# Optimization experiments

Measured on AMD Instinct MI355X. Metric: run time of the kernel, lower is better.

## Reference

```python
import jax, jax.numpy as jnp
import numpy as np
import math


def setup_inputs() -> dict:
    key0 = jax.random.key(0)
    kq, kk, kv = jax.random.split(key0, 3)
    B, H, L, S, D = 2, 8, 2048, 2048, 64
    query = jax.random.normal(kq, (B, H, L, D), dtype=jnp.float32)
    key = jax.random.normal(kk, (B, H, S, D), dtype=jnp.float32)
    value = jax.random.normal(kv, (B, H, S, D), dtype=jnp.float32)
    return {"query": query, "key": key, "value": value}


def reference(query, key, value):
    # SDPA with last=True, attn_mask=None, is_causal=False, dropout_p=0.0,
    # hook_fn is a side-effect callback whose return value is unused -> no-op.
    D = query.shape[-1]
    scale_factor = 1.0 / math.sqrt(D)
    # [B, H, L, S] attention scores
    attn_weight = jnp.einsum("bhld,bhsd->bhls", query, key) * scale_factor
    # last=True branch: self-similarity softmaxes of q and k
    q_attn = jnp.einsum("bhld,bhmd->bhlm", query, query) * scale_factor
    k_attn = jnp.einsum("bhsd,bhtd->bhst", key, key) * scale_factor
    output_attn_weight = jax.nn.softmax(q_attn, axis=-1) + jax.nn.softmax(k_attn, axis=-1)
    attn_weight = jax.nn.softmax(attn_weight, axis=-1)
    # dropout_p = 0.0 -> identity
    out = jnp.einsum("bhls,bhsd->bhld", attn_weight, value)
    return (out, output_attn_weight)
```

## Files before the change

### kernel.cpp

```cpp
#include <hip/hip_runtime.h>
#include <hip/hip_bf16.h>

#define LL 2048
#define DD 64

typedef __attribute__((ext_vector_type(4))) float f32x4;
typedef __attribute__((ext_vector_type(8))) short short8;
typedef __attribute__((ext_vector_type(4))) short short4v;

#define S1 0.18033688011112042f
#define S2 23.083120654223414f

static __device__ __forceinline__ short f2bf(float f) {
    union { float f; unsigned u; } v; v.f = f;
    unsigned r = v.u + 0x7fffu + ((v.u >> 16) & 1u);
    return (short)(r >> 16);
}

__global__ __launch_bounds__(256)
void prep_cvt(const float* __restrict__ Q, const float* __restrict__ K,
              short* __restrict__ Qb, short* __restrict__ Kb) {
    const float* src = blockIdx.y ? K : Q;
    short* dst = blockIdx.y ? Kb : Qb;
    size_t i = ((size_t)blockIdx.x * 256 + threadIdx.x) * 4;
    f32x4 v = *(const f32x4*)(src + i);
    short4v o;
    o[0] = f2bf(v[0]); o[1] = f2bf(v[1]); o[2] = f2bf(v[2]); o[3] = f2bf(v[3]);
    *(short4v*)(dst + i) = o;
}

__global__ __launch_bounds__(256)
void prep_vt(const float* __restrict__ V, short* __restrict__ Vt) {
    const int bh = blockIdx.y;
    const int s0 = blockIdx.x * 64;
    const int sl = threadIdx.x & 63;
    const int d0 = threadIdx.x >> 6;
    const float* Vs = V + (size_t)bh * LL * DD;
    short* Vd = Vt + (size_t)bh * DD * LL;
#pragma unroll
    for (int i = 0; i < 16; ++i) {
        int d = d0 + i * 4;
        Vd[(size_t)d * LL + s0 + sl] = f2bf(Vs[(size_t)(s0 + sl) * DD + d]);
    }
}


__global__ __launch_bounds__(512, 4)
void attnw_sums(const short* __restrict__ Qb, const short* __restrict__ Kb,
                float* __restrict__ Ssum) {
    const int bh = blockIdx.y;
    const int mat = blockIdx.z;
    const int r0 = blockIdx.x * 128;
    const int tid = threadIdx.x;
    const int lane = tid & 63;
    const int wid = tid >> 6;
    const int q = lane >> 4;
    const int c0 = lane & 15;

    __shared__ short8 stg[512];

    const short* X = (mat ? Kb : Qb) + (size_t)bh * LL * DD;
    float* Sd = Ssum + ((size_t)mat * 16 + bh) * LL;

    const int rw = r0 + wid * 16;
    const short8 a0 = *(const short8*)(X + (size_t)(rw + c0) * DD + q * 8);
    const short8 a1 = *(const short8*)(X + (size_t)(rw + c0) * DD + 32 + q * 8);

    const int sc = tid >> 3;
    const int sd = tid & 7;
    const int sslot = sc * 8 + (sd ^ (sc & 7));

    float sum[4] = {0.f, 0.f, 0.f, 0.f};
    short8 rst = *(const short8*)(X + (size_t)sc * DD + sd * 8);
    for (int i = 0; i < 32; ++i) {
        __syncthreads();
        stg[sslot] = rst;
        __syncthreads();
        if (i + 1 < 32)
            rst = *(const short8*)(X + (size_t)((i + 1) * 64 + sc) * DD + sd * 8);
#pragma unroll
        for (int h = 0; h < 4; ++h) {
            const int col = h * 16 + c0;
            short8 b0 = stg[col * 8 + (q ^ (c0 & 7))];
            short8 b1 = stg[col * 8 + ((q + 4) ^ (c0 & 7))];
            f32x4 z = {0.f, 0.f, 0.f, 0.f};
            z = __builtin_amdgcn_mfma_f32_16x16x32_bf16(a0, b0, z, 0, 0, 0);
            z = __builtin_amdgcn_mfma_f32_16x16x32_bf16(a1, b1, z, 0, 0, 0);
#pragma unroll
            for (int r = 0; r < 4; ++r)
                sum[r] += __builtin_amdgcn_exp2f(z[r] * S1 - S2);
        }
    }
#pragma unroll
    for (int off = 1; off < 16; off <<= 1)
#pragma unroll
        for (int r = 0; r < 4; ++r) sum[r] += __shfl_xor(sum[r], off, 64);
    if (c0 == 0) {
#pragma unroll
        for (int r = 0; r < 4; ++r) Sd[rw + q * 4 + r] = sum[r];
    }
}

__global__ __launch_bounds__(256, 4)
void attnw_write(const short* __restrict__ Qb, const short* __restrict__ Kb,
                 const float* __restrict__ Ssum, float* __restrict__ out2) {
    const int bh = blockIdx.y;
    const int r0 = blockIdx.x * 64;
    const int tid = threadIdx.x;
    const int lane = tid & 63;
    const int wid = tid >> 6;
    const int q = lane >> 4;
    const int c0 = lane & 15;

    __shared__ short8 stgQ[256];
    __shared__ short8 stgK[256];
    __shared__ __align__(16) float ob[4][16][36];

    const short* Qh = Qb + (size_t)bh * LL * DD;
    const short* Kh = Kb + (size_t)bh * LL * DD;
    const float* Sq = Ssum + (size_t)bh * LL;
    const float* Sk = Ssum + (size_t)(16 + bh) * LL;

    const int rw = r0 + wid * 16;
    const short8 aq0 = *(const short8*)(Qh + (size_t)(rw + c0) * DD + q * 8);
    const short8 aq1 = *(const short8*)(Qh + (size_t)(rw + c0) * DD + 32 + q * 8);
    const short8 ak0 = *(const short8*)(Kh + (size_t)(rw + c0) * DD + q * 8);
    const short8 ak1 = *(const short8*)(Kh + (size_t)(rw + c0) * DD + 32 + q * 8);

    float rclQ[4], rclK[4];
#pragma unroll
    for (int r = 0; r < 4; ++r) {
        rclQ[r] = 1.0f / Sq[rw + q * 4 + r];
        rclK[r] = 1.0f / Sk[rw + q * 4 + r];
    }

    const int sc = tid >> 3;
    const int sd = tid & 7;
    const int sslot = sc * 8 + (sd ^ (sc & 7));

    float* outp = out2 + (size_t)bh * LL * LL + (size_t)rw * LL;

    short8 rq = *(const short8*)(Qh + (size_t)sc * DD + sd * 8);
    short8 rk = *(const short8*)(Kh + (size_t)sc * DD + sd * 8);
    for (int i = 0; i < 64; ++i) {
        __syncthreads();
        stgQ[sslot] = rq;
        stgK[sslot] = rk;
        __syncthreads();
        if (i + 1 < 64) {
            rq = *(const short8*)(Qh + (size_t)((i + 1) * 32 + sc) * DD + sd * 8);
            rk = *(const short8*)(Kh + (size_t)((i + 1) * 32 + sc) * DD + sd * 8);
        }
#pragma unroll
        for (int h = 0; h < 2; ++h) {
            const int col = h * 16 + c0;
            short8 bq0 = stgQ[col * 8 + (q ^ (c0 & 7))];
            short8 bq1 = stgQ[col * 8 + ((q + 4) ^ (c0 & 7))];
            short8 bk0 = stgK[col * 8 + (q ^ (c0 & 7))];
            short8 bk1 = stgK[col * 8 + ((q + 4) ^ (c0 & 7))];
            f32x4 zq = {0.f, 0.f, 0.f, 0.f}, zk = {0.f, 0.f, 0.f, 0.f};
            zq = __builtin_amdgcn_mfma_f32_16x16x32_bf16(aq0, bq0, zq, 0, 0, 0);
            zq = __builtin_amdgcn_mfma_f32_16x16x32_bf16(aq1, bq1, zq, 0, 0, 0);
            zk = __builtin_amdgcn_mfma_f32_16x16x32_bf16(ak0, bk0, zk, 0, 0, 0);
            zk = __builtin_amdgcn_mfma_f32_16x16x32_bf16(ak1, bk1, zk, 0, 0, 0);
#pragma unroll
            for (int r = 0; r < 4; ++r) {
                float v = __builtin_amdgcn_exp2f(zq[r] * S1 - S2) * rclQ[r]
                        + __builtin_amdgcn_exp2f(zk[r] * S1 - S2) * rclK[r];
                ob[wid][q * 4 + r][h * 16 + c0] = v;
            }
        }
#pragma unroll
        for (int j = 0; j < 2; ++j) {
            int idx = lane + j * 64;
            int row = idx >> 3;
            int c8 = idx & 7;
            f32x4 v = *(const f32x4*)(&ob[wid][row][c8 * 4]);
            __builtin_nontemporal_store(
                v, (f32x4*)&outp[(size_t)row * LL + i * 32 + c8 * 4]);
        }
    }
}

__global__ __launch_bounds__(256, 4)
void sdpa_kernel(const short* __restrict__ Qb, const short* __restrict__ Kb,
                 const short* __restrict__ Vt, float* __restrict__ out1) {
    const int bh = blockIdx.y;
    const int r0 = blockIdx.x * 16;
    const int tid = threadIdx.x;
    const int lane = tid & 63;
    const int cw = tid >> 6;
    const int q = lane >> 4;
    const int c0 = lane & 15;
    const int colbase = cw * 512;

    __shared__ float redsum[4][16];
    __shared__ __align__(16) short pbuf[4][16][40];
    __shared__ float obuf[4][1024];

    const short* Qh = Qb + (size_t)bh * LL * DD;
    const short* Kh = Kb + (size_t)bh * LL * DD;
    const short* Vh = Vt + (size_t)bh * DD * LL;

    const short8 a0 = *(const short8*)(Qh + (size_t)(r0 + c0) * DD + q * 8);
    const short8 a1 = *(const short8*)(Qh + (size_t)(r0 + c0) * DD + 32 + q * 8);

    f32x4 oacc[4];
#pragma unroll
    for (int dt = 0; dt < 4; ++dt) { f32x4 z = {0.f,0.f,0.f,0.f}; oacc[dt] = z; }
    float sum[4] = {0.f, 0.f, 0.f, 0.f};

#pragma unroll 4
    for (int sb = 0; sb < 16; ++sb) {
        const int sglob = colbase + sb * 32;
#pragma unroll
        for (int h = 0; h < 2; ++h) {
            const short* Bp = Kh + (size_t)(sglob + h * 16 + c0) * DD + q * 8;
            short8 b0 = *(const short8*)Bp;
            short8 b1 = *(const short8*)(Bp + 32);
            f32x4 z = {0.f, 0.f, 0.f, 0.f};
            z = __builtin_amdgcn_mfma_f32_16x16x32_bf16(a0, b0, z, 0, 0, 0);
            z = __builtin_amdgcn_mfma_f32_16x16x32_bf16(a1, b1, z, 0, 0, 0);
#pragma unroll
            for (int r = 0; r < 4; ++r) {
                float e = __builtin_amdgcn_exp2f(z[r] * S1);
                sum[r] += e;
                pbuf[cw][q * 4 + r][h * 16 + c0] = f2bf(e);
            }
        }
        short8 ap = *(const short8*)(&pbuf[cw][c0][q * 8]);
#pragma unroll
        for (int dt = 0; dt < 4; ++dt) {
            short8 bv = *(const short8*)(Vh + (size_t)(dt * 16 + c0) * LL + sglob + q * 8);
            oacc[dt] = __builtin_amdgcn_mfma_f32_16x16x32_bf16(ap, bv, oacc[dt], 0, 0, 0);
        }
    }

#pragma unroll
    for (int off = 1; off < 16; off <<= 1)
#pragma unroll
        for (int r = 0; r < 4; ++r) sum[r] += __shfl_xor(sum[r], off, 64);
    if (c0 == 0) {
#pragma unroll
        for (int r = 0; r < 4; ++r) redsum[cw][q * 4 + r] = sum[r];
    }
    __syncthreads();
    float rcl[4];
#pragma unroll
    for (int r = 0; r < 4; ++r) {
        int rr = q * 4 + r;
        rcl[r] = 1.0f / (redsum[0][rr] + redsum[1][rr] + redsum[2][rr] + redsum[3][rr]);
    }

#pragma unroll
    for (int dt = 0; dt < 4; ++dt)
#pragma unroll
        for (int r = 0; r < 4; ++r)
            obuf[cw][(q * 4 + r) * 64 + dt * 16 + c0] = oacc[dt][r] * rcl[r];
    __syncthreads();
    float* o1 = out1 + (size_t)bh * LL * DD + (size_t)r0 * DD;
    {
        int e4 = tid;
        f32x4 v = *(const f32x4*)(&obuf[0][e4 * 4]);
        f32x4 v1 = *(const f32x4*)(&obuf[1][e4 * 4]);
        f32x4 v2 = *(const f32x4*)(&obuf[2][e4 * 4]);
        f32x4 v3 = *(const f32x4*)(&obuf[3][e4 * 4]);
        v = v + v1 + v2 + v3;
        *(f32x4*)(o1 + e4 * 4) = v;
    }
}

extern "C" void kernel_launch(void* const* d_in, const int* in_sizes, int n_in,
                              void* d_out, int out_size, void* d_ws, size_t ws_size,
                              hipStream_t stream) {
    const float* Q = (const float*)d_in[0];
    const float* K = (const float*)d_in[1];
    const float* V = (const float*)d_in[2];
    float* out1 = (float*)d_out;
    float* out2 = out1 + (size_t)16 * LL * DD;

    const size_t N = (size_t)16 * LL * DD;
    short* Qb = (short*)d_ws;
    short* Kb = Qb + N;
    short* Vt = Kb + N;

    float* Ssum = out1;

    prep_cvt<<<dim3((unsigned)(N / 1024), 2), 256, 0, stream>>>(Q, K, Qb, Kb);
    prep_vt<<<dim3(LL / 64, 16), 256, 0, stream>>>(V, Vt);

    attnw_sums<<<dim3(LL / 128, 16, 2), 512, 0, stream>>>(Qb, Kb, Ssum);
    attnw_write<<<dim3(LL / 64, 16), 256, 0, stream>>>(Qb, Kb, Ssum, out2);
    sdpa_kernel<<<dim3(LL / 16, 16), 256, 0, stream>>>(Qb, Kb, Vt, out1);
}
```

Before: 455.9 us.

## Restructure SDPA kernel: 64 rows per block with shared K/V staging

Each block now handles 64 query rows, one 16-row slab per wave, and all four waves sweep the full key range. Previously the four waves of a block split the key columns for 16 rows. K and V tiles of 32 keys are staged once per block into XOR-swizzled shared memory, with register prefetch of the next tile, so all four waves reuse them instead of each reading from global memory. This removes the cross-wave row-sum reduction and the summing of partial outputs, at the cost of two barriers per tile and a grid four times smaller.

```diff
diff --git a/kernel.cpp b/kernel.cpp
--- a/kernel.cpp
+++ b/kernel.cpp
@@ -186,15 +186,15 @@
 void sdpa_kernel(const short* __restrict__ Qb, const short* __restrict__ Kb,
                  const short* __restrict__ Vt, float* __restrict__ out1) {
     const int bh = blockIdx.y;
-    const int r0 = blockIdx.x * 16;
+    const int r0 = blockIdx.x * 64;
     const int tid = threadIdx.x;
     const int lane = tid & 63;
-    const int cw = tid >> 6;
+    const int wid = tid >> 6;
     const int q = lane >> 4;
     const int c0 = lane & 15;
-    const int colbase = cw * 512;
-
-    __shared__ float redsum[4][16];
+
+    __shared__ short8 stgK[256];
+    __shared__ short8 stgV[256];
     __shared__ __align__(16) short pbuf[4][16][40];
     __shared__ float obuf[4][1024];
 
@@ -202,22 +202,39 @@
     const short* Kh = Kb + (size_t)bh * LL * DD;
     const short* Vh = Vt + (size_t)bh * DD * LL;
 
-    const short8 a0 = *(const short8*)(Qh + (size_t)(r0 + c0) * DD + q * 8);
-    const short8 a1 = *(const short8*)(Qh + (size_t)(r0 + c0) * DD + 32 + q * 8);
+    const int rw = r0 + wid * 16;
+    const short8 a0 = *(const short8*)(Qh + (size_t)(rw + c0) * DD + q * 8);
+    const short8 a1 = *(const short8*)(Qh + (size_t)(rw + c0) * DD + 32 + q * 8);
 
     f32x4 oacc[4];
 #pragma unroll
     for (int dt = 0; dt < 4; ++dt) { f32x4 z = {0.f,0.f,0.f,0.f}; oacc[dt] = z; }
     float sum[4] = {0.f, 0.f, 0.f, 0.f};
 
-#pragma unroll 4
-    for (int sb = 0; sb < 16; ++sb) {
-        const int sglob = colbase + sb * 32;
+    const int sc = tid >> 3;
+    const int sdo = tid & 7;
+    const int kslot = sc * 8 + (sdo ^ (sc & 7));
+    const int vd = tid >> 2;
+    const int vs = tid & 3;
+    const int vslot = vd * 4 + (vs ^ (vd & 3));
+
+    short8 rk = *(const short8*)(Kh + (size_t)sc * DD + sdo * 8);
+    short8 rv = *(const short8*)(Vh + (size_t)vd * LL + vs * 8);
+
+    for (int i = 0; i < 64; ++i) {
+        __syncthreads();
+        stgK[kslot] = rk;
+        stgV[vslot] = rv;
+        __syncthreads();
+        if (i + 1 < 64) {
+            rk = *(const short8*)(Kh + (size_t)((i + 1) * 32 + sc) * DD + sdo * 8);
+            rv = *(const short8*)(Vh + (size_t)vd * LL + (i + 1) * 32 + vs * 8);
+        }
 #pragma unroll
         for (int h = 0; h < 2; ++h) {
-            const short* Bp = Kh + (size_t)(sglob + h * 16 + c0) * DD + q * 8;
-            short8 b0 = *(const short8*)Bp;
-            short8 b1 = *(const short8*)(Bp + 32);
+            const int col = h * 16 + c0;
+            short8 b0 = stgK[col * 8 + (q ^ (col & 7))];
+            short8 b1 = stgK[col * 8 + ((q + 4) ^ (col & 7))];
             f32x4 z = {0.f, 0.f, 0.f, 0.f};
             z = __builtin_amdgcn_mfma_f32_16x16x32_bf16(a0, b0, z, 0, 0, 0);
             z = __builtin_amdgcn_mfma_f32_16x16x32_bf16(a1, b1, z, 0, 0, 0);
@@ -225,13 +242,14 @@
             for (int r = 0; r < 4; ++r) {
                 float e = __builtin_amdgcn_exp2f(z[r] * S1);
                 sum[r] += e;
-                pbuf[cw][q * 4 + r][h * 16 + c0] = f2bf(e);
+                pbuf[wid][q * 4 + r][h * 16 + c0] = f2bf(e);
             }
         }
-        short8 ap = *(const short8*)(&pbuf[cw][c0][q * 8]);
+        short8 ap = *(const short8*)(&pbuf[wid][c0][q * 8]);
 #pragma unroll
         for (int dt = 0; dt < 4; ++dt) {
-            short8 bv = *(const short8*)(Vh + (size_t)(dt * 16 + c0) * LL + sglob + q * 8);
+            const int d = dt * 16 + c0;
+            short8 bv = stgV[d * 4 + (q ^ (d & 3))];
             oacc[dt] = __builtin_amdgcn_mfma_f32_16x16x32_bf16(ap, bv, oacc[dt], 0, 0, 0);
         }
     }
@@ -240,32 +258,20 @@
     for (int off = 1; off < 16; off <<= 1)
 #pragma unroll
         for (int r = 0; r < 4; ++r) sum[r] += __shfl_xor(sum[r], off, 64);
-    if (c0 == 0) {
-#pragma unroll
-        for (int r = 0; r < 4; ++r) redsum[cw][q * 4 + r] = sum[r];
-    }
-    __syncthreads();
     float rcl[4];
 #pragma unroll
-    for (int r = 0; r < 4; ++r) {
-        int rr = q * 4 + r;
-        rcl[r] = 1.0f / (redsum[0][rr] + redsum[1][rr] + redsum[2][rr] + redsum[3][rr]);
-    }
+    for (int r = 0; r < 4; ++r) rcl[r] = 1.0f / sum[r];
 
 #pragma unroll
     for (int dt = 0; dt < 4; ++dt)
 #pragma unroll
         for (int r = 0; r < 4; ++r)
-            obuf[cw][(q * 4 + r) * 64 + dt * 16 + c0] = oacc[dt][r] * rcl[r];
-    __syncthreads();
-    float* o1 = out1 + (size_t)bh * LL * DD + (size_t)r0 * DD;
-    {
-        int e4 = tid;
-        f32x4 v = *(const f32x4*)(&obuf[0][e4 * 4]);
-        f32x4 v1 = *(const f32x4*)(&obuf[1][e4 * 4]);
-        f32x4 v2 = *(const f32x4*)(&obuf[2][e4 * 4]);
-        f32x4 v3 = *(const f32x4*)(&obuf[3][e4 * 4]);
-        v = v + v1 + v2 + v3;
+            obuf[wid][(q * 4 + r) * 64 + dt * 16 + c0] = oacc[dt][r] * rcl[r];
+    float* o1 = out1 + (size_t)bh * LL * DD + (size_t)rw * DD;
+#pragma unroll
+    for (int j = 0; j < 4; ++j) {
+        int e4 = lane + j * 64;
+        f32x4 v = *(const f32x4*)(&obuf[wid][e4 * 4]);
         *(f32x4*)(o1 + e4 * 4) = v;
     }
 }
@@ -291,5 +297,5 @@
 
     attnw_sums<<<dim3(LL / 128, 16, 2), 512, 0, stream>>>(Qb, Kb, Ssum);
     attnw_write<<<dim3(LL / 64, 16), 256, 0, stream>>>(Qb, Kb, Ssum, out2);
-    sdpa_kernel<<<dim3(LL / 16, 16), 256, 0, stream>>>(Qb, Kb, Vt, out1);
-}
+    sdpa_kernel<<<dim3(LL / 64, 16), 256, 0, stream>>>(Qb, Kb, Vt, out1);
+}
```

Measured after the change: 388.1 us. 14.9% less time.
